# Optimization experiments

Hardware: AMD Instinct MI355X
Metric: run time of the kernel (lower is better)

The kernel has to match this reference:

```python
import jax, jax.numpy as jnp
import numpy as np

N_NODES = 50000
D_IN = 64
HID = 64
OUT = 64
NEG_SLOPE = 0.2


def setup_inputs() -> dict:
    key = jax.random.key(0)
    ks = jax.random.split(key, 16)
    s = 1.0 / np.sqrt(D_IN)
    inp = {
        "x": jax.random.normal(ks[0], (N_NODES, D_IN), dtype=jnp.float32),
        "edge_index": jax.random.randint(ks[1], (2, 1200000), 0, N_NODES, dtype=jnp.int64),
        # conv1 (GATConv, heads=1): separate src/dst projections + attention vectors + bias
        "W1_src": jax.random.uniform(ks[2], (D_IN, HID), jnp.float32, -s, s),
        "W1_dst": jax.random.uniform(ks[3], (D_IN, HID), jnp.float32, -s, s),
        "att1_src": jax.random.uniform(ks[4], (HID,), jnp.float32, -s, s),
        "att1_dst": jax.random.uniform(ks[5], (HID,), jnp.float32, -s, s),
        "b1": jnp.zeros((HID,), jnp.float32),
        # lin1 residual
        "Wl1": jax.random.uniform(ks[6], (D_IN, HID), jnp.float32, -s, s),
        "bl1": jnp.zeros((HID,), jnp.float32),
        # conv2
        "W2_src": jax.random.uniform(ks[7], (HID, OUT), jnp.float32, -s, s),
        "W2_dst": jax.random.uniform(ks[8], (HID, OUT), jnp.float32, -s, s),
        "att2_src": jax.random.uniform(ks[9], (OUT,), jnp.float32, -s, s),
        "att2_dst": jax.random.uniform(ks[10], (OUT,), jnp.float32, -s, s),
        "b2": jnp.zeros((OUT,), jnp.float32),
        # lin2 residual
        "Wl2": jax.random.uniform(ks[11], (HID, OUT), jnp.float32, -s, s),
        "bl2": jnp.zeros((OUT,), jnp.float32),
    }
    return inp


def _gat_conv(x, W_src, W_dst, att_src, att_dst, bias, src, dst, n_nodes):
    # project nodes: [N, C]
    h_src = x @ W_src
    h_dst = x @ W_dst
    # per-node attention logits: [N]
    a_src = h_src @ att_src
    a_dst = h_dst @ att_dst
    # per-edge score, leaky relu (slope 0.2)
    e = a_src[src] + a_dst[dst]  # [E]
    e = jnp.where(e >= 0, e, NEG_SLOPE * e)
    # segment softmax over incoming edges of each dst node
    seg_max = jax.lax.stop_gradient(
        jax.ops.segment_max(e, dst, num_segments=n_nodes))  # [N]
    w = jnp.exp(e - seg_max[dst])  # [E]
    seg_sum = jax.ops.segment_sum(w, dst, num_segments=n_nodes)  # [N]
    alpha = w / seg_sum[dst]  # [E]
    # weighted scatter-add of gathered src features
    msg = h_src[src] * alpha[:, None]  # [E, C]
    out = jax.ops.segment_sum(msg, dst, num_segments=n_nodes)  # [N, C]
    return out + bias


def reference(x, edge_index, W1_src, W1_dst, att1_src, att1_dst, b1, Wl1, bl1,
              W2_src, W2_dst, att2_src, att2_dst, b2, Wl2, bl2):
    src, dst = edge_index[0], edge_index[1]
    n = x.shape[0]
    h = _gat_conv(x, W1_src, W1_dst, att1_src, att1_dst, b1, src, dst, n)
    h = jax.nn.relu(h + x @ Wl1 + bl1)
    o = _gat_conv(h, W2_src, W2_dst, att2_src, att2_dst, b2, src, dst, n)
    o = jax.nn.relu(o + h @ Wl2 + bl2)
    return o
```

## Files before the change

### kernel.cpp

```cpp
#include <hip/hip_runtime.h>
#include <hip/hip_fp16.h>

#define NEG 0.2f
#define BSHIFT 9
#define BNODES 512
#define ECAP 14336

typedef _Float16 half8_t __attribute__((ext_vector_type(8)));
typedef float   floatx4_t __attribute__((ext_vector_type(4)));
typedef float   floatx2_t __attribute__((ext_vector_type(2)));

__device__ __forceinline__ void agg_core(
    int beg, int end, float ad, int lane, int g, int l,
    const int* __restrict__ ssrc, const float* __restrict__ asrc,
    const unsigned* __restrict__ h4,
    float& a0, float& a1, float& a2, float& a3, float& sumw) {
    a0 = a1 = a2 = a3 = sumw = 0.f;
    while (beg < end) {
        int nb = min(64, end - beg);
        int s_l = 0; float w_l = 0.f;
        if (lane < nb) {
            s_l = ssrc[beg + lane];
            float e = asrc[s_l] + ad;
            e = (e >= 0.f) ? e : NEG * e;
            w_l = __expf(e);
        }
        int i = 0;
        for (; i + 15 < nb; i += 16) {
            int iA = i + g, iB = i + 4 + g, iC = i + 8 + g, iD = i + 12 + g;
            int   sA = __shfl(s_l, iA, 64), sB = __shfl(s_l, iB, 64);
            int   sC = __shfl(s_l, iC, 64), sD = __shfl(s_l, iD, 64);
            float wA = __shfl(w_l, iA, 64), wB = __shfl(w_l, iB, 64);
            float wC = __shfl(w_l, iC, 64), wD = __shfl(w_l, iD, 64);
            unsigned vA = h4[(size_t)sA * 16 + l];
            unsigned vB = h4[(size_t)sB * 16 + l];
            unsigned vC = h4[(size_t)sC * 16 + l];
            unsigned vD = h4[(size_t)sD * 16 + l];
            floatx2_t fA0 = __builtin_amdgcn_cvt_pk_f32_fp8(vA, false);
            floatx2_t fA1 = __builtin_amdgcn_cvt_pk_f32_fp8(vA, true);
            floatx2_t fB0 = __builtin_amdgcn_cvt_pk_f32_fp8(vB, false);
            floatx2_t fB1 = __builtin_amdgcn_cvt_pk_f32_fp8(vB, true);
            floatx2_t fC0 = __builtin_amdgcn_cvt_pk_f32_fp8(vC, false);
            floatx2_t fC1 = __builtin_amdgcn_cvt_pk_f32_fp8(vC, true);
            floatx2_t fD0 = __builtin_amdgcn_cvt_pk_f32_fp8(vD, false);
            floatx2_t fD1 = __builtin_amdgcn_cvt_pk_f32_fp8(vD, true);
            sumw += (wA + wB) + (wC + wD);
            a0 += wA * fA0.x + wB * fB0.x + wC * fC0.x + wD * fD0.x;
            a1 += wA * fA0.y + wB * fB0.y + wC * fC0.y + wD * fD0.y;
            a2 += wA * fA1.x + wB * fB1.x + wC * fC1.x + wD * fD1.x;
            a3 += wA * fA1.y + wB * fB1.y + wC * fC1.y + wD * fD1.y;
        }
        for (; i + 7 < nb; i += 8) {
            int iA = i + g, iB = i + 4 + g;
            int   sA = __shfl(s_l, iA, 64), sB = __shfl(s_l, iB, 64);
            float wA = __shfl(w_l, iA, 64), wB = __shfl(w_l, iB, 64);
            unsigned vA = h4[(size_t)sA * 16 + l];
            unsigned vB = h4[(size_t)sB * 16 + l];
            floatx2_t fA0 = __builtin_amdgcn_cvt_pk_f32_fp8(vA, false);
            floatx2_t fA1 = __builtin_amdgcn_cvt_pk_f32_fp8(vA, true);
            floatx2_t fB0 = __builtin_amdgcn_cvt_pk_f32_fp8(vB, false);
            floatx2_t fB1 = __builtin_amdgcn_cvt_pk_f32_fp8(vB, true);
            sumw += wA + wB;
            a0 += wA * fA0.x + wB * fB0.x;
            a1 += wA * fA0.y + wB * fB0.y;
            a2 += wA * fA1.x + wB * fB1.x;
            a3 += wA * fA1.y + wB * fB1.y;
        }
        for (; i < nb; i += 4) {
            int iA = i + g;
            int   sA = __shfl(s_l, iA, 64);
            float wA = __shfl(w_l, iA, 64);
            unsigned vA = h4[(size_t)sA * 16 + l];
            floatx2_t fA0 = __builtin_amdgcn_cvt_pk_f32_fp8(vA, false);
            floatx2_t fA1 = __builtin_amdgcn_cvt_pk_f32_fp8(vA, true);
            sumw += wA;
            a0 += wA * fA0.x; a1 += wA * fA0.y;
            a2 += wA * fA1.x; a3 += wA * fA1.y;
        }
        beg += nb;
    }
    a0 += __shfl_xor(a0, 16, 64); a0 += __shfl_xor(a0, 32, 64);
    a1 += __shfl_xor(a1, 16, 64); a1 += __shfl_xor(a1, 32, 64);
    a2 += __shfl_xor(a2, 16, 64); a2 += __shfl_xor(a2, 32, 64);
    a3 += __shfl_xor(a3, 16, 64); a3 += __shfl_xor(a3, 32, 64);
    sumw += __shfl_xor(sumw, 16, 64); sumw += __shfl_xor(sumw, 32, 64);
}

__global__ __launch_bounds__(256) void bin_prep(
    const int* __restrict__ src, const int* __restrict__ dst,
    int* __restrict__ gcur, unsigned* __restrict__ binned, int E, int K,
    const float* __restrict__ W1s, const float* __restrict__ a1s,
    const float* __restrict__ W1d, const float* __restrict__ a1d,
    const float* __restrict__ W2s, const float* __restrict__ a2s,
    const float* __restrict__ W2d, const float* __restrict__ a2d,
    const float* __restrict__ Wl1, const float* __restrict__ Wl2,
    __half* __restrict__ wf) {
    int t = threadIdx.x;
    if (blockIdx.x == gridDim.x - 1) {
        __shared__ float vsm[256];
        {
            int g = t >> 6, k = t & 63;
            const float* W = (g == 0) ? W1s : (g == 1) ? W1d : (g == 2) ? W2s : W2d;
            const float* a = (g == 0) ? a1s : (g == 1) ? a1d : (g == 2) ? a2s : a2d;
            float s = 0.f;
            #pragma unroll 8
            for (int j = 0; j < 64; ++j) s += W[k * 64 + j] * a[j];
            vsm[t] = s;
        }
        __syncthreads();
        __half* wS1 = wf;
        __half* wL1 = wf + 4096;
        __half* wV1 = wf + 8192;
        __half* wS2 = wf + 9216;
        __half* wL2 = wf + 13312;
        __half* wV2 = wf + 17408;
        for (int e = t; e < 4096; e += 256) {
            int j = e & 7, ln = (e >> 3) & 63, tile = e >> 9;
            int nt = tile >> 1, kt = tile & 1;
            int kk = kt * 32 + ((ln >> 4) << 3) + j;
            int nn = (nt << 4) + (ln & 15);
            int wi = kk * 64 + nn;
            wS1[e] = __float2half(W1s[wi]);
            wL1[e] = __float2half(Wl1[wi]);
            wS2[e] = __float2half(W2s[wi]);
            wL2[e] = __float2half(Wl2[wi]);
        }
        for (int e = t; e < 1024; e += 256) {
            int j = e & 7, ln = (e >> 3) & 63, kt = e >> 9;
            int kk = kt * 32 + ((ln >> 4) << 3) + j;
            int nn = ln & 15;
            float v1 = (nn == 0) ? vsm[kk] : (nn == 1) ? vsm[64 + kk] : 0.f;
            float v2 = (nn == 0) ? vsm[128 + kk] : (nn == 1) ? vsm[192 + kk] : 0.f;
            wV1[e] = __float2half(v1);
            wV2[e] = __float2half(v2);
        }
        return;
    }
    __shared__ int h[128], cbase[128], cur[128];
    if (t < 128) h[t] = 0;
    __syncthreads();
    int base = blockIdx.x * 2048;
    #pragma unroll
    for (int i = 0; i < 8; ++i) {
        int idx = base + i * 256 + t;
        if (idx < E) atomicAdd(&h[dst[idx] >> BSHIFT], 1);
    }
    __syncthreads();
    if (t < K) {
        cbase[t] = t * ECAP + (h[t] ? atomicAdd(&gcur[t], h[t]) : 0);
        cur[t] = 0;
    }
    __syncthreads();
    #pragma unroll
    for (int i = 0; i < 8; ++i) {
        int idx = base + i * 256 + t;
        if (idx < E) {
            int d = dst[idx], s = src[idx];
            int b = d >> BSHIFT;
            int pos = cbase[b] + atomicAdd(&cur[b], 1);
            binned[pos] = ((unsigned)s << BSHIFT) | (unsigned)(d & (BNODES - 1));
        }
    }
}

__device__ __forceinline__ void mfma_tile(
    int tid, int row0, int rows,
    _Float16* xh, float* xf,
    const __half* wsF, const __half* wlF, const __half* wvF,
    const float* __restrict__ bconv, const float* __restrict__ blin,
    unsigned* __restrict__ hsrc8, float* __restrict__ base_out,
    float* __restrict__ asrc, float* __restrict__ adst) {
    int w = tid >> 6, lane = tid & 63, m = lane & 15, q = lane >> 4;
    half8_t a0 = *(const half8_t*)&xh[(w * 16 + m) * 72 + q * 8];
    half8_t a1 = *(const half8_t*)&xh[(w * 16 + m) * 72 + 32 + q * 8];
    const half8_t* bS = (const half8_t*)(const void*)wsF;
    const half8_t* bL = (const half8_t*)(const void*)wlF;
    const half8_t* bV = (const half8_t*)(const void*)wvF;
    floatx4_t z = {0.f, 0.f, 0.f, 0.f};
    floatx4_t cs[4], cl[4], cv;
    #pragma unroll
    for (int nt = 0; nt < 4; ++nt) {
        cs[nt] = __builtin_amdgcn_mfma_f32_16x16x32_f16(a0, bS[(nt * 2 + 0) * 64 + lane], z, 0, 0, 0);
        cs[nt] = __builtin_amdgcn_mfma_f32_16x16x32_f16(a1, bS[(nt * 2 + 1) * 64 + lane], cs[nt], 0, 0, 0);
        cl[nt] = __builtin_amdgcn_mfma_f32_16x16x32_f16(a0, bL[(nt * 2 + 0) * 64 + lane], z, 0, 0, 0);
        cl[nt] = __builtin_amdgcn_mfma_f32_16x16x32_f16(a1, bL[(nt * 2 + 1) * 64 + lane], cl[nt], 0, 0, 0);
    }
    cv = __builtin_amdgcn_mfma_f32_16x16x32_f16(a0, bV[lane], z, 0, 0, 0);
    cv = __builtin_amdgcn_mfma_f32_16x16x32_f16(a1, bV[64 + lane], cv, 0, 0, 0);
    __syncthreads();
    #pragma unroll
    for (int nt = 0; nt < 4; ++nt)
        #pragma unroll
        for (int r = 0; r < 4; ++r)
            xf[(w * 16 + q * 4 + r) * 68 + nt * 16 + m] = cs[nt][r];
    __syncthreads();
    #pragma unroll
    for (int i = 0; i < 2; ++i) {
        int u = tid + i * 256;
        int r = u >> 3, c8 = (u & 7) * 8;
        if (r < rows) {
            float4 v0 = *(const float4*)&xf[r * 68 + c8];
            float4 v1 = *(const float4*)&xf[r * 68 + c8 + 4];
            int lo = __builtin_amdgcn_cvt_pk_fp8_f32(v0.x, v0.y, 0, false);
            lo = __builtin_amdgcn_cvt_pk_fp8_f32(v0.z, v0.w, lo, true);
            int hi = __builtin_amdgcn_cvt_pk_fp8_f32(v1.x, v1.y, 0, false);
            hi = __builtin_amdgcn_cvt_pk_fp8_f32(v1.z, v1.w, hi, true);
            uint2 pk; pk.x = (unsigned)lo; pk.y = (unsigned)hi;
            *(uint2*)&hsrc8[(size_t)(row0 + r) * 16 + (u & 7) * 2] = pk;
        }
    }
    __syncthreads();
    float bb[4];
    bb[0] = bconv[m] + blin[m];
    bb[1] = bconv[16 + m] + blin[16 + m];
    bb[2] = bconv[32 + m] + blin[32 + m];
    bb[3] = bconv[48 + m] + blin[48 + m];
    #pragma unroll
    for (int nt = 0; nt < 4; ++nt)
        #pragma unroll
        for (int r = 0; r < 4; ++r)
            xf[(w * 16 + q * 4 + r) * 68 + nt * 16 + m] = cl[nt][r] + bb[nt];
    __syncthreads();
    #pragma unroll
    for (int i = 0; i < 4; ++i) {
        int u = tid + i * 256;
        int r = u >> 4, c4 = (u & 15) * 4;
        if (r < rows)
            *(float4*)&base_out[(size_t)(row0 + r) * 64 + c4] = *(const float4*)&xf[r * 68 + c4];
    }
    int rb = w * 16 + q * 4;
    if (m == 0) {
        #pragma unroll
        for (int r = 0; r < 4; ++r)
            if (rb + r < rows) asrc[row0 + rb + r] = cv[r];
    } else if (m == 1) {
        #pragma unroll
        for (int r = 0; r < 4; ++r)
            if (rb + r < rows) adst[row0 + rb + r] = cv[r];
    }
}

__global__ __launch_bounds__(256) void csr_gemm(
    const unsigned* __restrict__ binned, int* __restrict__ ssrc,
    const int* __restrict__ gcur, int* __restrict__ rowbeg, int* __restrict__ rowend,
    const float* __restrict__ x, const __half* __restrict__ wsF,
    const __half* __restrict__ wlF, const __half* __restrict__ wvF,
    const float* __restrict__ bconv, const float* __restrict__ blin,
    unsigned* __restrict__ hsrc8, float* __restrict__ base_out,
    float* __restrict__ asrc, float* __restrict__ adst, int N, int K) {
    __shared__ union {
        struct { int lh[512]; int ps[256]; } c;
        _Float16 xh[64 * 72];
        float    xf[64 * 68];
    } sm;
    int tid = threadIdx.x;
    int blk = blockIdx.x;

    if (blk < K) {
        int base = blk * ECAP;
        int cnt = min(gcur[blk], ECAP);
        sm.c.lh[tid] = 0; sm.c.lh[tid + 256] = 0;
        __syncthreads();
        for (int i = tid; i < cnt; i += 256)
            atomicAdd(&sm.c.lh[binned[base + i] & (BNODES - 1)], 1);
        __syncthreads();
        int a0 = sm.c.lh[2 * tid], a1 = sm.c.lh[2 * tid + 1];
        sm.c.ps[tid] = a0 + a1;
        __syncthreads();
        for (int off = 1; off < 256; off <<= 1) {
            int v = (tid >= off) ? sm.c.ps[tid - off] : 0;
            __syncthreads();
            sm.c.ps[tid] += v;
            __syncthreads();
        }
        int exc = sm.c.ps[tid] - (a0 + a1);
        int node0 = blk * BNODES + 2 * tid, node1 = node0 + 1;
        if (node0 < N) { rowbeg[node0] = base + exc;      rowend[node0] = base + exc + a0; }
        if (node1 < N) { rowbeg[node1] = base + exc + a0; rowend[node1] = base + exc + a0 + a1; }
        __syncthreads();
        sm.c.lh[2 * tid] = exc; sm.c.lh[2 * tid + 1] = exc + a0;
        __syncthreads();
        for (int i = tid; i < cnt; i += 256) {
            unsigned e = binned[base + i];
            int pos = atomicAdd(&sm.c.lh[e & (BNODES - 1)], 1);
            ssrc[base + pos] = (int)(e >> BSHIFT);
        }
        return;
    }

    int gb = blk - K;
    int row0 = gb * 64;
    int rows = min(64, N - row0);
    #pragma unroll
    for (int i = 0; i < 4; ++i) {
        int u = tid + i * 256;
        int r = u >> 4, c4 = (u & 15) * 4;
        if (r < rows) {
            float4 v = *(const float4*)&x[(size_t)(row0 + r) * 64 + c4];
            *(__half2*)&sm.xh[r * 72 + c4]     = __floats2half2_rn(v.x, v.y);
            *(__half2*)&sm.xh[r * 72 + c4 + 2] = __floats2half2_rn(v.z, v.w);
        }
    }
    __syncthreads();
    mfma_tile(tid, row0, rows, sm.xh, sm.xf, wsF, wlF, wvF,
              bconv, blin, hsrc8, base_out, asrc, adst);
}

__global__ __launch_bounds__(256) void node_gemm2(
    const __half* __restrict__ xh_in, const __half* __restrict__ wsF,
    const __half* __restrict__ wlF, const __half* __restrict__ wvF,
    const float* __restrict__ bconv, const float* __restrict__ blin,
    unsigned* __restrict__ hsrc8, float* __restrict__ base_out,
    float* __restrict__ asrc, float* __restrict__ adst, int N) {
    __shared__ union {
        _Float16 xh[64 * 72];
        float    xf[64 * 68];
    } sm;
    int tid = threadIdx.x;
    int row0 = blockIdx.x * 64;
    int rows = min(64, N - row0);
    #pragma unroll
    for (int i = 0; i < 2; ++i) {
        int u = tid + i * 256;
        int r = u >> 3, c8 = (u & 7) * 8;
        if (r < rows)
            *(float4*)&sm.xh[r * 72 + c8] =
                *(const float4*)&xh_in[(size_t)(row0 + r) * 64 + c8];
    }
    __syncthreads();
    mfma_tile(tid, row0, rows, sm.xh, sm.xf, wsF, wlF, wvF,
              bconv, blin, hsrc8, base_out, asrc, adst);
}

__global__ __launch_bounds__(256) void gat_aggregate_h(
    const int* __restrict__ rowbeg, const int* __restrict__ rowend,
    const int* __restrict__ ssrc,
    const float* __restrict__ asrc, const float* __restrict__ adst,
    const unsigned* __restrict__ h4, const float* __restrict__ base,
    __half2* __restrict__ out, int N) {
    int d = blockIdx.x * 4 + (threadIdx.x >> 6);
    int lane = threadIdx.x & 63, g = lane >> 4, l = lane & 15;
    if (d >= N) return;
    float a0, a1, a2, a3, sw;
    agg_core(rowbeg[d], rowend[d], adst[d], lane, g, l, ssrc, asrc, h4,
             a0, a1, a2, a3, sw);
    if (g == 0) {
        float4 b4 = *(const float4*)&base[(size_t)d * 64 + 4 * l];
        float invw = (sw > 0.f) ? 1.f / sw : 0.f;
        float2 pk;
        ((__half2*)&pk)[0] = __floats2half2_rn(fmaxf(b4.x + a0 * invw, 0.f),
                                               fmaxf(b4.y + a1 * invw, 0.f));
        ((__half2*)&pk)[1] = __floats2half2_rn(fmaxf(b4.z + a2 * invw, 0.f),
                                               fmaxf(b4.w + a3 * invw, 0.f));
        *(float2*)&out[(size_t)d * 32 + 2 * l] = pk;
    }
}

__global__ __launch_bounds__(256) void gat_aggregate_f(
    const int* __restrict__ rowbeg, const int* __restrict__ rowend,
    const int* __restrict__ ssrc,
    const float* __restrict__ asrc, const float* __restrict__ adst,
    const unsigned* __restrict__ h4, const float* __restrict__ base,
    float* __restrict__ out, int N) {
    int d = blockIdx.x * 4 + (threadIdx.x >> 6);
    int lane = threadIdx.x & 63, g = lane >> 4, l = lane & 15;
    if (d >= N) return;
    float a0, a1, a2, a3, sw;
    agg_core(rowbeg[d], rowend[d], adst[d], lane, g, l, ssrc, asrc, h4,
             a0, a1, a2, a3, sw);
    if (g == 0) {
        float4 b4 = *(const float4*)&base[(size_t)d * 64 + 4 * l];
        float invw = (sw > 0.f) ? 1.f / sw : 0.f;
        float4 o;
        o.x = fmaxf(b4.x + a0 * invw, 0.f);
        o.y = fmaxf(b4.y + a1 * invw, 0.f);
        o.z = fmaxf(b4.z + a2 * invw, 0.f);
        o.w = fmaxf(b4.w + a3 * invw, 0.f);
        *(float4*)&out[(size_t)d * 64 + 4 * l] = o;
    }
}

extern "C" void kernel_launch(void* const* d_in, const int* in_sizes, int n_in,
                              void* d_out, int out_size, void* d_ws, size_t ws_size,
                              hipStream_t stream) {
    const float* x    = (const float*)d_in[0];
    const int*   ei   = (const int*)d_in[1];
    const float* W1s  = (const float*)d_in[2];
    const float* W1d  = (const float*)d_in[3];
    const float* a1s  = (const float*)d_in[4];
    const float* a1d  = (const float*)d_in[5];
    const float* b1   = (const float*)d_in[6];
    const float* Wl1  = (const float*)d_in[7];
    const float* bl1  = (const float*)d_in[8];
    const float* W2s  = (const float*)d_in[9];
    const float* W2d  = (const float*)d_in[10];
    const float* a2s  = (const float*)d_in[11];
    const float* a2d  = (const float*)d_in[12];
    const float* b2   = (const float*)d_in[13];
    const float* Wl2  = (const float*)d_in[14];
    const float* bl2  = (const float*)d_in[15];

    const int N = in_sizes[0] / 64;
    const int E = in_sizes[1] / 2;
    const int* src = ei;
    const int* dst = ei + E;
    const int K = (N + BNODES - 1) >> BSHIFT;

    float* ws = (float*)d_ws;
    size_t o = 0;
    unsigned* hsrc8 = (unsigned*)(ws + o); o += (size_t)N * 16;
    __half2* hmidH  = (__half2*)(ws + o); o += (size_t)N * 32;
    float* base   = ws + o; o += (size_t)N * 64;
    float* asrc   = ws + o; o += N;
    float* adst   = ws + o; o += N;
    __half* wf    = (__half*)(ws + o); o += 9216;
    int* rowbeg = (int*)(ws + o); o += N;
    int* rowend = (int*)(ws + o); o += N;
    int* gcur   = (int*)(ws + o); o += 128;
    unsigned* binned = (unsigned*)(ws + o); o += (size_t)K * ECAP;
    int* ssrc   = (int*)(ws + o); o += (size_t)K * ECAP;

    const __half* wS1 = wf;
    const __half* wL1 = wf + 4096;
    const __half* wV1 = wf + 8192;
    const __half* wS2 = wf + 9216;
    const __half* wL2 = wf + 13312;
    const __half* wV2 = wf + 17408;

    const int EB = (E + 2047) / 2048;
    const int GB = (N + 63) / 64;

    (void)hipMemsetAsync(gcur, 0, 128 * sizeof(int), stream);
    bin_prep<<<EB + 1, 256, 0, stream>>>(src, dst, gcur, binned, E, K,
                                         W1s, a1s, W1d, a1d, W2s, a2s, W2d, a2d,
                                         Wl1, Wl2, wf);

    csr_gemm<<<K + GB, 256, 0, stream>>>(
        binned, ssrc, gcur, rowbeg, rowend,
        x, wS1, wL1, wV1, b1, bl1,
        hsrc8, base, asrc, adst, N, K);

    gat_aggregate_h<<<(N + 3) / 4, 256, 0, stream>>>(
        rowbeg, rowend, ssrc, asrc, adst, hsrc8, base, hmidH, N);

    node_gemm2<<<GB, 256, 0, stream>>>((const __half*)hmidH, wS2, wL2, wV2,
                                       b2, bl2, hsrc8, base, asrc, adst, N);

    gat_aggregate_f<<<(N + 3) / 4, 256, 0, stream>>>(
        rowbeg, rowend, ssrc, asrc, adst, hsrc8, base,
        (float*)d_out, N);
}
```

Before: 211.1 us.

## Replace two-pass bucket binning with global per-node histogram, scan, atomic scatter

Builds the CSR directly: a global atomic histogram of in-degree per destination node, a per-bucket scan to get row offsets, then an atomic-cursor scatter of source ids into their rows. This drops the intermediate binned array and the per-bucket local counting-sort pass, saving a full read and write of the edge list. In exchange it adds one more kernel launch and relies on many global atomics spread across 50k counters, which can contend and produce a non-deterministic edge order within each row. It also assumes no bucket overflows ECAP.

```diff
diff --git a/kernel.cpp b/kernel.cpp
--- a/kernel.cpp
+++ b/kernel.cpp
@@ -86,9 +86,8 @@
     sumw += __shfl_xor(sumw, 16, 64); sumw += __shfl_xor(sumw, 32, 64);
 }
 
-__global__ __launch_bounds__(256) void bin_prep(
-    const int* __restrict__ src, const int* __restrict__ dst,
-    int* __restrict__ gcur, unsigned* __restrict__ binned, int E, int K,
+__global__ __launch_bounds__(256) void hist_prep(
+    const int* __restrict__ dst, int* __restrict__ rowend, int E,
     const float* __restrict__ W1s, const float* __restrict__ a1s,
     const float* __restrict__ W1d, const float* __restrict__ a1d,
     const float* __restrict__ W2s, const float* __restrict__ a2s,
@@ -136,31 +135,33 @@
         }
         return;
     }
-    __shared__ int h[128], cbase[128], cur[128];
-    if (t < 128) h[t] = 0;
-    __syncthreads();
     int base = blockIdx.x * 2048;
     #pragma unroll
     for (int i = 0; i < 8; ++i) {
         int idx = base + i * 256 + t;
-        if (idx < E) atomicAdd(&h[dst[idx] >> BSHIFT], 1);
-    }
-    __syncthreads();
-    if (t < K) {
-        cbase[t] = t * ECAP + (h[t] ? atomicAdd(&gcur[t], h[t]) : 0);
-        cur[t] = 0;
-    }
-    __syncthreads();
-    #pragma unroll
-    for (int i = 0; i < 8; ++i) {
-        int idx = base + i * 256 + t;
-        if (idx < E) {
-            int d = dst[idx], s = src[idx];
-            int b = d >> BSHIFT;
-            int pos = cbase[b] + atomicAdd(&cur[b], 1);
-            binned[pos] = ((unsigned)s << BSHIFT) | (unsigned)(d & (BNODES - 1));
-        }
-    }
+        if (idx < E) atomicAdd(&rowend[dst[idx]], 1);
+    }
+}
+
+__global__ __launch_bounds__(256) void bucket_scan(
+    int* __restrict__ rowbeg, int* __restrict__ rowend, int N) {
+    __shared__ int ps[256];
+    int t = threadIdx.x;
+    int n0 = blockIdx.x * BNODES + 2 * t, n1 = n0 + 1;
+    int d0 = (n0 < N) ? rowend[n0] : 0;
+    int d1 = (n1 < N) ? rowend[n1] : 0;
+    ps[t] = d0 + d1;
+    __syncthreads();
+    for (int off = 1; off < 256; off <<= 1) {
+        int v = (t >= off) ? ps[t - off] : 0;
+        __syncthreads();
+        ps[t] += v;
+        __syncthreads();
+    }
+    int exc = ps[t] - (d0 + d1);
+    int base = blockIdx.x * ECAP;
+    if (n0 < N) { rowbeg[n0] = base + exc;      rowend[n0] = base + exc; }
+    if (n1 < N) { rowbeg[n1] = base + exc + d0; rowend[n1] = base + exc + d0; }
 }
 
 __device__ __forceinline__ void mfma_tile(
@@ -240,55 +241,36 @@
     }
 }
 
-__global__ __launch_bounds__(256) void csr_gemm(
-    const unsigned* __restrict__ binned, int* __restrict__ ssrc,
-    const int* __restrict__ gcur, int* __restrict__ rowbeg, int* __restrict__ rowend,
+__global__ __launch_bounds__(256) void scatter_gemm(
+    const int* __restrict__ src, const int* __restrict__ dst,
+    int* __restrict__ rowend, int* __restrict__ ssrc, int E, int SB,
     const float* __restrict__ x, const __half* __restrict__ wsF,
     const __half* __restrict__ wlF, const __half* __restrict__ wvF,
     const float* __restrict__ bconv, const float* __restrict__ blin,
     unsigned* __restrict__ hsrc8, float* __restrict__ base_out,
-    float* __restrict__ asrc, float* __restrict__ adst, int N, int K) {
+    float* __restrict__ asrc, float* __restrict__ adst, int N) {
+    int tid = threadIdx.x;
+    int blk = blockIdx.x;
+
+    if (blk < SB) {
+        int base = blk * 2048;
+        #pragma unroll
+        for (int i = 0; i < 8; ++i) {
+            int idx = base + i * 256 + tid;
+            if (idx < E) {
+                int d = dst[idx], s = src[idx];
+                int pos = atomicAdd(&rowend[d], 1);
+                ssrc[pos] = s;
+            }
+        }
+        return;
+    }
+
     __shared__ union {
-        struct { int lh[512]; int ps[256]; } c;
         _Float16 xh[64 * 72];
         float    xf[64 * 68];
     } sm;
-    int tid = threadIdx.x;
-    int blk = blockIdx.x;
-
-    if (blk < K) {
-        int base = blk * ECAP;
-        int cnt = min(gcur[blk], ECAP);
-        sm.c.lh[tid] = 0; sm.c.lh[tid + 256] = 0;
-        __syncthreads();
-        for (int i = tid; i < cnt; i += 256)
-            atomicAdd(&sm.c.lh[binned[base + i] & (BNODES - 1)], 1);
-        __syncthreads();
-        int a0 = sm.c.lh[2 * tid], a1 = sm.c.lh[2 * tid + 1];
-        sm.c.ps[tid] = a0 + a1;
-        __syncthreads();
-        for (int off = 1; off < 256; off <<= 1) {
-            int v = (tid >= off) ? sm.c.ps[tid - off] : 0;
-            __syncthreads();
-            sm.c.ps[tid] += v;
-            __syncthreads();
-        }
-        int exc = sm.c.ps[tid] - (a0 + a1);
-        int node0 = blk * BNODES + 2 * tid, node1 = node0 + 1;
-        if (node0 < N) { rowbeg[node0] = base + exc;      rowend[node0] = base + exc + a0; }
-        if (node1 < N) { rowbeg[node1] = base + exc + a0; rowend[node1] = base + exc + a0 + a1; }
-        __syncthreads();
-        sm.c.lh[2 * tid] = exc; sm.c.lh[2 * tid + 1] = exc + a0;
-        __syncthreads();
-        for (int i = tid; i < cnt; i += 256) {
-            unsigned e = binned[base + i];
-            int pos = atomicAdd(&sm.c.lh[e & (BNODES - 1)], 1);
-            ssrc[base + pos] = (int)(e >> BSHIFT);
-        }
-        return;
-    }
-
-    int gb = blk - K;
+    int gb = blk - SB;
     int row0 = gb * 64;
     int rows = min(64, N - row0);
     #pragma unroll
@@ -416,8 +398,6 @@
     __half* wf    = (__half*)(ws + o); o += 9216;
     int* rowbeg = (int*)(ws + o); o += N;
     int* rowend = (int*)(ws + o); o += N;
-    int* gcur   = (int*)(ws + o); o += 128;
-    unsigned* binned = (unsigned*)(ws + o); o += (size_t)K * ECAP;
     int* ssrc   = (int*)(ws + o); o += (size_t)K * ECAP;
 
     const __half* wS1 = wf;
@@ -430,15 +410,17 @@
     const int EB = (E + 2047) / 2048;
     const int GB = (N + 63) / 64;
 
-    (void)hipMemsetAsync(gcur, 0, 128 * sizeof(int), stream);
-    bin_prep<<<EB + 1, 256, 0, stream>>>(src, dst, gcur, binned, E, K,
-                                         W1s, a1s, W1d, a1d, W2s, a2s, W2d, a2d,
-                                         Wl1, Wl2, wf);
-
-    csr_gemm<<<K + GB, 256, 0, stream>>>(
-        binned, ssrc, gcur, rowbeg, rowend,
+    (void)hipMemsetAsync(rowend, 0, (size_t)N * sizeof(int), stream);
+    hist_prep<<<EB + 1, 256, 0, stream>>>(dst, rowend, E,
+                                          W1s, a1s, W1d, a1d, W2s, a2s, W2d, a2d,
+                                          Wl1, Wl2, wf);
+
+    bucket_scan<<<K, 256, 0, stream>>>(rowbeg, rowend, N);
+
+    scatter_gemm<<<EB + GB, 256, 0, stream>>>(
+        src, dst, rowend, ssrc, E, EB,
         x, wS1, wL1, wV1, b1, bl1,
-        hsrc8, base, asrc, adst, N, K);
+        hsrc8, base, asrc, adst, N);
 
     gat_aggregate_h<<<(N + 3) / 4, 256, 0, stream>>>(
         rowbeg, rowend, ssrc, asrc, adst, hsrc8, base, hmidH, N);
```

New measurement: 296.7 us. 1.41x slower.

## Aggregate each destination node with a 16-lane group instead of a full wave

Applied to the files above, without the earlier changes.

The aggregation kernels now map one destination node to 16 lanes rather than 64, so each wave handles four nodes. Each lane walks the node's edge list sequentially, computing the attention weight itself and loading its 4-byte fp8 slice of the source row, with 4-way unrolling. This removes the cross-lane shuffles, the final xor reductions and the three idle quarter-waves during the epilogue, and it uses more of the wave when degrees are small (about 24 on average). In exchange, the 16 lanes of a group recompute the same edge weight redundantly, edges are no longer spread across the wave, and load imbalance between nodes that share a wave can rise.

```diff
diff --git a/kernel.cpp b/kernel.cpp
--- a/kernel.cpp
+++ b/kernel.cpp
@@ -10,80 +10,52 @@
 typedef float   floatx4_t __attribute__((ext_vector_type(4)));
 typedef float   floatx2_t __attribute__((ext_vector_type(2)));
 
-__device__ __forceinline__ void agg_core(
-    int beg, int end, float ad, int lane, int g, int l,
+__device__ __forceinline__ void agg16(
+    int beg, int end, float ad, int l,
     const int* __restrict__ ssrc, const float* __restrict__ asrc,
     const unsigned* __restrict__ h4,
     float& a0, float& a1, float& a2, float& a3, float& sumw) {
     a0 = a1 = a2 = a3 = sumw = 0.f;
-    while (beg < end) {
-        int nb = min(64, end - beg);
-        int s_l = 0; float w_l = 0.f;
-        if (lane < nb) {
-            s_l = ssrc[beg + lane];
-            float e = asrc[s_l] + ad;
-            e = (e >= 0.f) ? e : NEG * e;
-            w_l = __expf(e);
-        }
-        int i = 0;
-        for (; i + 15 < nb; i += 16) {
-            int iA = i + g, iB = i + 4 + g, iC = i + 8 + g, iD = i + 12 + g;
-            int   sA = __shfl(s_l, iA, 64), sB = __shfl(s_l, iB, 64);
-            int   sC = __shfl(s_l, iC, 64), sD = __shfl(s_l, iD, 64);
-            float wA = __shfl(w_l, iA, 64), wB = __shfl(w_l, iB, 64);
-            float wC = __shfl(w_l, iC, 64), wD = __shfl(w_l, iD, 64);
-            unsigned vA = h4[(size_t)sA * 16 + l];
-            unsigned vB = h4[(size_t)sB * 16 + l];
-            unsigned vC = h4[(size_t)sC * 16 + l];
-            unsigned vD = h4[(size_t)sD * 16 + l];
-            floatx2_t fA0 = __builtin_amdgcn_cvt_pk_f32_fp8(vA, false);
-            floatx2_t fA1 = __builtin_amdgcn_cvt_pk_f32_fp8(vA, true);
-            floatx2_t fB0 = __builtin_amdgcn_cvt_pk_f32_fp8(vB, false);
-            floatx2_t fB1 = __builtin_amdgcn_cvt_pk_f32_fp8(vB, true);
-            floatx2_t fC0 = __builtin_amdgcn_cvt_pk_f32_fp8(vC, false);
-            floatx2_t fC1 = __builtin_amdgcn_cvt_pk_f32_fp8(vC, true);
-            floatx2_t fD0 = __builtin_amdgcn_cvt_pk_f32_fp8(vD, false);
-            floatx2_t fD1 = __builtin_amdgcn_cvt_pk_f32_fp8(vD, true);
-            sumw += (wA + wB) + (wC + wD);
-            a0 += wA * fA0.x + wB * fB0.x + wC * fC0.x + wD * fD0.x;
-            a1 += wA * fA0.y + wB * fB0.y + wC * fC0.y + wD * fD0.y;
-            a2 += wA * fA1.x + wB * fB1.x + wC * fC1.x + wD * fD1.x;
-            a3 += wA * fA1.y + wB * fB1.y + wC * fC1.y + wD * fD1.y;
-        }
-        for (; i + 7 < nb; i += 8) {
-            int iA = i + g, iB = i + 4 + g;
-            int   sA = __shfl(s_l, iA, 64), sB = __shfl(s_l, iB, 64);
-            float wA = __shfl(w_l, iA, 64), wB = __shfl(w_l, iB, 64);
-            unsigned vA = h4[(size_t)sA * 16 + l];
-            unsigned vB = h4[(size_t)sB * 16 + l];
-            floatx2_t fA0 = __builtin_amdgcn_cvt_pk_f32_fp8(vA, false);
-            floatx2_t fA1 = __builtin_amdgcn_cvt_pk_f32_fp8(vA, true);
-            floatx2_t fB0 = __builtin_amdgcn_cvt_pk_f32_fp8(vB, false);
-            floatx2_t fB1 = __builtin_amdgcn_cvt_pk_f32_fp8(vB, true);
-            sumw += wA + wB;
-            a0 += wA * fA0.x + wB * fB0.x;
-            a1 += wA * fA0.y + wB * fB0.y;
-            a2 += wA * fA1.x + wB * fB1.x;
-            a3 += wA * fA1.y + wB * fB1.y;
-        }
-        for (; i < nb; i += 4) {
-            int iA = i + g;
-            int   sA = __shfl(s_l, iA, 64);
-            float wA = __shfl(w_l, iA, 64);
-            unsigned vA = h4[(size_t)sA * 16 + l];
-            floatx2_t fA0 = __builtin_amdgcn_cvt_pk_f32_fp8(vA, false);
-            floatx2_t fA1 = __builtin_amdgcn_cvt_pk_f32_fp8(vA, true);
-            sumw += wA;
-            a0 += wA * fA0.x; a1 += wA * fA0.y;
-            a2 += wA * fA1.x; a3 += wA * fA1.y;
-        }
-        beg += nb;
-    }
-    a0 += __shfl_xor(a0, 16, 64); a0 += __shfl_xor(a0, 32, 64);
-    a1 += __shfl_xor(a1, 16, 64); a1 += __shfl_xor(a1, 32, 64);
-    a2 += __shfl_xor(a2, 16, 64); a2 += __shfl_xor(a2, 32, 64);
-    a3 += __shfl_xor(a3, 16, 64); a3 += __shfl_xor(a3, 32, 64);
-    sumw += __shfl_xor(sumw, 16, 64); sumw += __shfl_xor(sumw, 32, 64);
+    int e = beg;
+    for (; e + 3 < end; e += 4) {
+        int s0 = ssrc[e], s1 = ssrc[e + 1], s2 = ssrc[e + 2], s3 = ssrc[e + 3];
+        float x0 = asrc[s0] + ad, x1 = asrc[s1] + ad;
+        float x2 = asrc[s2] + ad, x3 = asrc[s3] + ad;
+        unsigned v0 = h4[(size_t)s0 * 16 + l];
+        unsigned v1 = h4[(size_t)s1 * 16 + l];
+        unsigned v2 = h4[(size_t)s2 * 16 + l];
+        unsigned v3 = h4[(size_t)s3 * 16 + l];
+        x0 = (x0 >= 0.f) ? x0 : NEG * x0;
+        x1 = (x1 >= 0.f) ? x1 : NEG * x1;
+        x2 = (x2 >= 0.f) ? x2 : NEG * x2;
+        x3 = (x3 >= 0.f) ? x3 : NEG * x3;
+        float w0 = __expf(x0), w1 = __expf(x1), w2 = __expf(x2), w3 = __expf(x3);
+        floatx2_t f00 = __builtin_amdgcn_cvt_pk_f32_fp8(v0, false);
+        floatx2_t f01 = __builtin_amdgcn_cvt_pk_f32_fp8(v0, true);
+        floatx2_t f10 = __builtin_amdgcn_cvt_pk_f32_fp8(v1, false);
+        floatx2_t f11 = __builtin_amdgcn_cvt_pk_f32_fp8(v1, true);
+        floatx2_t f20 = __builtin_amdgcn_cvt_pk_f32_fp8(v2, false);
+        floatx2_t f21 = __builtin_amdgcn_cvt_pk_f32_fp8(v2, true);
+        floatx2_t f30 = __builtin_amdgcn_cvt_pk_f32_fp8(v3, false);
+        floatx2_t f31 = __builtin_amdgcn_cvt_pk_f32_fp8(v3, true);
+        sumw += (w0 + w1) + (w2 + w3);
+        a0 += w0 * f00.x + w1 * f10.x + w2 * f20.x + w3 * f30.x;
+        a1 += w0 * f00.y + w1 * f10.y + w2 * f20.y + w3 * f30.y;
+        a2 += w0 * f01.x + w1 * f11.x + w2 * f21.x + w3 * f31.x;
+        a3 += w0 * f01.y + w1 * f11.y + w2 * f21.y + w3 * f31.y;
+    }
+    for (; e < end; ++e) {
+        int s = ssrc[e];
+        float x = asrc[s] + ad;
+        unsigned v = h4[(size_t)s * 16 + l];
+        x = (x >= 0.f) ? x : NEG * x;
+        float w = __expf(x);
+        floatx2_t f0 = __builtin_amdgcn_cvt_pk_f32_fp8(v, false);
+        floatx2_t f1 = __builtin_amdgcn_cvt_pk_f32_fp8(v, true);
+        sumw += w;
+        a0 += w * f0.x; a1 += w * f0.y;
+        a2 += w * f1.x; a3 += w * f1.y;
+    }
 }
 
 __global__ __launch_bounds__(256) void bin_prep(
@@ -338,22 +310,20 @@
     const float* __restrict__ asrc, const float* __restrict__ adst,
     const unsigned* __restrict__ h4, const float* __restrict__ base,
     __half2* __restrict__ out, int N) {
-    int d = blockIdx.x * 4 + (threadIdx.x >> 6);
-    int lane = threadIdx.x & 63, g = lane >> 4, l = lane & 15;
+    int d = blockIdx.x * 16 + (threadIdx.x >> 4);
+    int l = threadIdx.x & 15;
     if (d >= N) return;
     float a0, a1, a2, a3, sw;
-    agg_core(rowbeg[d], rowend[d], adst[d], lane, g, l, ssrc, asrc, h4,
-             a0, a1, a2, a3, sw);
-    if (g == 0) {
-        float4 b4 = *(const float4*)&base[(size_t)d * 64 + 4 * l];
-        float invw = (sw > 0.f) ? 1.f / sw : 0.f;
-        float2 pk;
-        ((__half2*)&pk)[0] = __floats2half2_rn(fmaxf(b4.x + a0 * invw, 0.f),
-                                               fmaxf(b4.y + a1 * invw, 0.f));
-        ((__half2*)&pk)[1] = __floats2half2_rn(fmaxf(b4.z + a2 * invw, 0.f),
-                                               fmaxf(b4.w + a3 * invw, 0.f));
-        *(float2*)&out[(size_t)d * 32 + 2 * l] = pk;
-    }
+    agg16(rowbeg[d], rowend[d], adst[d], l, ssrc, asrc, h4,
+          a0, a1, a2, a3, sw);
+    float4 b4 = *(const float4*)&base[(size_t)d * 64 + 4 * l];
+    float invw = (sw > 0.f) ? 1.f / sw : 0.f;
+    float2 pk;
+    ((__half2*)&pk)[0] = __floats2half2_rn(fmaxf(b4.x + a0 * invw, 0.f),
+                                           fmaxf(b4.y + a1 * invw, 0.f));
+    ((__half2*)&pk)[1] = __floats2half2_rn(fmaxf(b4.z + a2 * invw, 0.f),
+                                           fmaxf(b4.w + a3 * invw, 0.f));
+    *(float2*)&out[(size_t)d * 32 + 2 * l] = pk;
 }
 
 __global__ __launch_bounds__(256) void gat_aggregate_f(
@@ -362,22 +332,20 @@
     const float* __restrict__ asrc, const float* __restrict__ adst,
     const unsigned* __restrict__ h4, const float* __restrict__ base,
     float* __restrict__ out, int N) {
-    int d = blockIdx.x * 4 + (threadIdx.x >> 6);
-    int lane = threadIdx.x & 63, g = lane >> 4, l = lane & 15;
+    int d = blockIdx.x * 16 + (threadIdx.x >> 4);
+    int l = threadIdx.x & 15;
     if (d >= N) return;
     float a0, a1, a2, a3, sw;
-    agg_core(rowbeg[d], rowend[d], adst[d], lane, g, l, ssrc, asrc, h4,
-             a0, a1, a2, a3, sw);
-    if (g == 0) {
-        float4 b4 = *(const float4*)&base[(size_t)d * 64 + 4 * l];
-        float invw = (sw > 0.f) ? 1.f / sw : 0.f;
-        float4 o;
-        o.x = fmaxf(b4.x + a0 * invw, 0.f);
-        o.y = fmaxf(b4.y + a1 * invw, 0.f);
-        o.z = fmaxf(b4.z + a2 * invw, 0.f);
-        o.w = fmaxf(b4.w + a3 * invw, 0.f);
-        *(float4*)&out[(size_t)d * 64 + 4 * l] = o;
-    }
+    agg16(rowbeg[d], rowend[d], adst[d], l, ssrc, asrc, h4,
+          a0, a1, a2, a3, sw);
+    float4 b4 = *(const float4*)&base[(size_t)d * 64 + 4 * l];
+    float invw = (sw > 0.f) ? 1.f / sw : 0.f;
+    float4 o;
+    o.x = fmaxf(b4.x + a0 * invw, 0.f);
+    o.y = fmaxf(b4.y + a1 * invw, 0.f);
+    o.z = fmaxf(b4.z + a2 * invw, 0.f);
+    o.w = fmaxf(b4.w + a3 * invw, 0.f);
+    *(float4*)&out[(size_t)d * 64 + 4 * l] = o;
 }
 
 extern "C" void kernel_launch(void* const* d_in, const int* in_sizes, int n_in,
@@ -429,6 +397,7 @@
 
     const int EB = (E + 2047) / 2048;
     const int GB = (N + 63) / 64;
+    const int AB = (N + 15) / 16;
 
     (void)hipMemsetAsync(gcur, 0, 128 * sizeof(int), stream);
     bin_prep<<<EB + 1, 256, 0, stream>>>(src, dst, gcur, binned, E, K,
@@ -440,13 +409,13 @@
         x, wS1, wL1, wV1, b1, bl1,
         hsrc8, base, asrc, adst, N, K);
 
-    gat_aggregate_h<<<(N + 3) / 4, 256, 0, stream>>>(
+    gat_aggregate_h<<<AB, 256, 0, stream>>>(
         rowbeg, rowend, ssrc, asrc, adst, hsrc8, base, hmidH, N);
 
     node_gemm2<<<GB, 256, 0, stream>>>((const __half*)hmidH, wS2, wL2, wV2,
                                        b2, bl2, hsrc8, base, asrc, adst, N);
 
-    gat_aggregate_f<<<(N + 3) / 4, 256, 0, stream>>>(
+    gat_aggregate_f<<<AB, 256, 0, stream>>>(
         rowbeg, rowend, ssrc, asrc, adst, hsrc8, base,
         (float*)d_out, N);
 }
```

Measured after the change: 207.1 us. Within noise of the previous version (-1.9%).
